# Performance work log

Measured on AMD Instinct MI355X. Metric: run time of the kernel, lower is better.

Reference implementation:

```python
import jax, jax.numpy as jnp
import numpy as np


def _forward(data_vecs, data_weights, data_biases, edge_weights, edge_biases,
             score_weights, data, types, graphs, edges, pos):
    data = np.asarray(data); types = np.asarray(types)
    graphs = np.asarray(graphs); edges = np.asarray(edges).copy()
    pos = int(pos)
    edges[pos] = -1  # forward() mutation: score the pos edge over ALL edge types
    n = int(data.shape[0]); G = int(graphs.shape[0]); dim = data_weights.shape[-1]

    # base (leaf) embeddings for all nodes at once: [n, dim]
    sel = data_vecs[types, data]  # [n, vec_dim] embedding-table gather
    base = jnp.einsum('nv,nvd->nd', sel, data_weights[types]) + data_biases[types]

    def add_child(emb, ce, e):
        # emb/ce: [dim] or [E, dim]; e < 0 -> broadcast child over all edge types
        if e < 0:
            contrib = jnp.einsum('d,edf->ef', ce, edge_weights) + edge_biases
        else:
            contrib = ce @ edge_weights[e] + edge_biases[e]
        return emb + contrib  # broadcasting [dim] + [E,dim] mirrors torch's cat-expand

    scores = []
    for g in range(G):
        parents = graphs[g].copy()
        roots = [i for i in range(n) if parents[i] == i]
        for i in range(len(roots) - 1):  # chain multiple roots (no-op for single root)
            parents[roots[i]] = roots[i + 1]
        root = roots[-1]
        parents[root] = -n
        children = {}
        for c in range(n):
            p = int(parents[c])
            if p >= 0:
                children.setdefault(p, []).append(c)
        denom = float(len(children) + 1)  # faithful to source: len of whole dict

        def rec(idx):
            emb = base[idx]
            if idx not in children:
                return emb
            for c in children[idx]:
                emb = add_child(emb, rec(c), int(edges[c]))
            return jnp.maximum(emb / denom, 0.0)

        emb = rec(root)
        final = add_child(jnp.zeros((dim,), base.dtype), emb, int(edges[root]))
        scores.append((final @ score_weights)[:, 0])  # [E]
    return jnp.stack(scores)  # [G, E]


def setup_inputs():
    T, V, VD, DIM, E = 2, 100000, 512, 512, 64
    N, G = 128, 16
    ks = jax.random.split(jax.random.key(0), 6)
    s = DIM ** -0.5  # keep recursion numerically stable (torch.rand init would overflow)
    inp = {
        'data_vecs': jax.random.normal(ks[0], (T, V, VD), jnp.float32),
        'data_weights': jax.random.uniform(ks[1], (T, VD, DIM), jnp.float32) * s,
        'data_biases': jax.random.uniform(ks[2], (T, DIM), jnp.float32) * s,
        'edge_weights': jax.random.uniform(ks[3], (E, DIM, DIM), jnp.float32) * s,
        'edge_biases': jax.random.uniform(ks[4], (E, DIM), jnp.float32) * s,
        'score_weights': jax.random.uniform(ks[5], (DIM, 1), jnp.float32) * s,
    }
    rng = np.random.RandomState(0)
    inp['data'] = rng.randint(0, V, size=N).astype(np.int64)
    inp['types'] = rng.randint(0, T, size=N).astype(np.int64)
    graphs = np.zeros((G, N), dtype=np.int64)
    for g in range(G):
        for i in range(1, N):
            graphs[g, i] = rng.randint(0, i)  # random tree; node 0 self-parent = root
    inp['graphs'] = graphs
    inp['edges'] = rng.randint(0, E, size=N).astype(np.int64)
    inp['pos'] = 5
    return inp


def reference(data_vecs, data_weights, data_biases, edge_weights, edge_biases,
              score_weights, data, types, graphs, edges, pos):
    return _forward(data_vecs, data_weights, data_biases, edge_weights,
                    edge_biases, score_weights, data, types, graphs, edges, pos)
```

## Files before the change

kernel.cpp:

```cpp
#include <hip/hip_runtime.h>

#define DIMC 512
#define NMAX 128

__global__ __launch_bounds__(256)
void base_kernel(const float* __restrict__ data_vecs,
                 const float* __restrict__ data_weights,
                 const float* __restrict__ data_biases,
                 const int* __restrict__ data,
                 const int* __restrict__ types,
                 float* __restrict__ base,
                 int V, int VD) {
  const int n = blockIdx.x;
  const int t = threadIdx.x;
  __shared__ float sel[DIMC];
  const int ty = types[n];
  const long long idx = data[n];
  const float* src = data_vecs + ((long long)ty * V + idx) * VD;
  for (int d = t; d < VD; d += 256) sel[d] = src[d];
  __syncthreads();
  const float* W = data_weights + (long long)ty * VD * DIMC;
  const int f0 = 2 * t;
  float2 a = {0.f, 0.f};
  for (int d = 0; d < VD; ++d) {
    const float s = sel[d];
    const float2 w = *(const float2*)(W + (long long)d * DIMC + f0);
    a.x = fmaf(s, w.x, a.x);
    a.y = fmaf(s, w.y, a.y);
  }
  const float* b = data_biases + (long long)ty * DIMC;
  base[(long long)n * DIMC + f0]     = a.x + b[f0];
  base[(long long)n * DIMC + f0 + 1] = a.y + b[f0 + 1];
}

__global__ __launch_bounds__(NMAX)
void setup_kernel(const int* __restrict__ graphs,
                  const int* __restrict__ edges,
                  const int* __restrict__ pos_p,
                  int* __restrict__ par, int* __restrict__ onp,
                  int* __restrict__ chOff, int* __restrict__ chList,
                  int* __restrict__ plist,
                  int* __restrict__ plen, int* __restrict__ eroot,
                  float* __restrict__ inv_denom,
                  int G, int N) {
  const int g = blockIdx.x;
  const int t = threadIdx.x;
  __shared__ int P[NMAX], C[NMAX], O[NMAX], CO[NMAX + 1];
  __shared__ int s_root;
  if (t < N) { P[t] = graphs[g * N + t]; C[t] = 0; O[t] = 0; }
  __syncthreads();
  if (t == 0) {
    int prev = -1;
    for (int i = 0; i < N; ++i)
      if (P[i] == i) { if (prev >= 0) P[prev] = i; prev = i; }
    s_root = prev;
    P[prev] = -1;
  }
  __syncthreads();
  const int root = s_root;
  if (t < N) { const int p = P[t]; if (p >= 0) atomicAdd(&C[p], 1); }
  __syncthreads();
  if (t == 0) {
    int internal = 0, acc = 0;
    for (int c = 0; c < N; ++c) {
      CO[c] = acc; acc += C[c];
      if (C[c] > 0) internal++;
    }
    CO[N] = acc;
    inv_denom[g] = 1.0f / (float)(internal + 1);
  }
  __syncthreads();
  if (t < N) {
    const int p = P[t];
    if (p >= 0) {
      int r = 0;
      for (int c = 0; c < t; ++c) if (P[c] == p) ++r;
      chList[g * N + CO[p] + r] = t;
    }
  }
  if (t == 0) {
    const int pos = *pos_p;
    int pl = 0;
    int x = (pos == root) ? -1 : P[pos];
    while (x >= 0) { plist[g * N + pl++] = x; O[x] = 1; x = P[x]; }
    plen[g] = pl;
    eroot[g] = (root == pos) ? -1 : edges[root];
  }
  __syncthreads();
  if (t < N) {
    par[g * N + t] = P[t];
    onp[g * N + t] = O[t];
    chOff[g * (N + 1) + t] = CO[t];
  }
  if (t == 0) chOff[g * (N + 1) + N] = CO[N];
}

__global__ __launch_bounds__(512)
void score_prep_kernel(const float* __restrict__ ew, const float* __restrict__ eb,
                       const float* __restrict__ sw_g,
                       const int* __restrict__ eroot,
                       float* __restrict__ u, float* __restrict__ c0) {
  const int g = blockIdx.x;
  const int t = threadIdx.x;
  __shared__ float sw[DIMC];
  __shared__ float red[DIMC];
  sw[t] = sw_g[t];
  __syncthreads();
  const int er = eroot[g];
  if (er < 0) { if (t == 0) c0[g] = 0.f; return; }
  const float* row = ew + (long long)er * DIMC * DIMC + (long long)t * DIMC;
  float a = 0.f;
  for (int f = 0; f < DIMC; ++f) a = fmaf(row[f], sw[f], a);
  u[(long long)g * DIMC + t] = a;
  red[t] = eb[(long long)er * DIMC + t] * sw[t];
  __syncthreads();
  for (int s = 256; s > 0; s >>= 1) {
    if (t < s) red[t] += red[t + s];
    __syncthreads();
  }
  if (t == 0) c0[g] = red[0];
}

__device__ __forceinline__ float agent_ld(const float* p) {
  return __hip_atomic_load((float*)p, __ATOMIC_RELAXED, __HIP_MEMORY_SCOPE_AGENT);
}
__device__ __forceinline__ void agent_st(float* p, float v) {
  __hip_atomic_store(p, v, __ATOMIC_RELAXED, __HIP_MEMORY_SCOPE_AGENT);
}

struct P1Args {
  const float* base; float* epos; float* contrib;
  const float* ew; const float* eb;
  const int* par; const int* onp;
  const int* chOff; const int* chList;
  const int* edges; const float* invd; const int* pos_p;
  int* ready;
  int G, N;
};

__global__ __launch_bounds__(128, 4)
void pass1_flags(P1Args p) {
  const int b = blockIdx.x;
  const int g = b / p.N;
  const int c = p.N - 1 - (b - g * p.N);
  const int gi = g * p.N + c;
  if (p.onp[gi]) return;
  const int t = threadIdx.x;
  const int f0 = 4 * t;
  __shared__ float v[DIMC];
  const int pos = *p.pos_p;
  const int pr = p.par[gi];
  const float inv = p.invd[g];
  const int cs   = p.chOff[g * (p.N + 1) + c];
  const int cend = p.chOff[g * (p.N + 1) + c + 1];

  if (cend > cs) {
    if (t == 0) {
      for (int k = cs; k < cend; ++k) {
        const int ch = p.chList[g * p.N + k];
        while (__hip_atomic_load(p.ready + (g * p.N + ch), __ATOMIC_RELAXED,
                                 __HIP_MEMORY_SCOPE_AGENT) == 0)
          __builtin_amdgcn_s_sleep(2);
      }
    }
    __syncthreads();
  }

  const float* bs = p.base + (long long)c * DIMC;
  float4 val = *(const float4*)(bs + f0);
  if (cend > cs) {
    for (int k = cs; k < cend; ++k) {
      const int ch = p.chList[g * p.N + k];
      const float* cv = p.contrib + ((long long)g * p.N + ch) * DIMC;
      val.x += agent_ld(cv + f0);
      val.y += agent_ld(cv + f0 + 1);
      val.z += agent_ld(cv + f0 + 2);
      val.w += agent_ld(cv + f0 + 3);
    }
    val.x = fmaxf(val.x * inv, 0.f);
    val.y = fmaxf(val.y * inv, 0.f);
    val.z = fmaxf(val.z * inv, 0.f);
    val.w = fmaxf(val.w * inv, 0.f);
  }
  if (c == pos)
    *(float4*)(p.epos + (long long)g * DIMC + f0) = val;
  v[f0] = val.x; v[f0 + 1] = val.y; v[f0 + 2] = val.z; v[f0 + 3] = val.w;
  __syncthreads();

  if (c != pos && pr >= 0) {
    const int e = p.edges[c];
    const float* W = p.ew + (long long)e * DIMC * DIMC;
    float4 a = {0.f, 0.f, 0.f, 0.f};
    #pragma unroll 8
    for (int d = 0; d < DIMC; ++d) {
      const float s = v[d];
      const float4 w = *(const float4*)(W + (long long)d * DIMC + f0);
      a.x = fmaf(s, w.x, a.x);
      a.y = fmaf(s, w.y, a.y);
      a.z = fmaf(s, w.z, a.z);
      a.w = fmaf(s, w.w, a.w);
    }
    const float4 bb = *(const float4*)(p.eb + (long long)e * DIMC + f0);
    float* cv = p.contrib + ((long long)g * p.N + c) * DIMC;
    agent_st(cv + f0,     a.x + bb.x);
    agent_st(cv + f0 + 1, a.y + bb.y);
    agent_st(cv + f0 + 2, a.z + bb.z);
    agent_st(cv + f0 + 3, a.w + bb.w);
  }
  __syncthreads();
  if (t == 0) {
    asm volatile("s_waitcnt vmcnt(0)" ::: "memory");
    __hip_atomic_store(p.ready + gi, 1, __ATOMIC_RELAXED,
                       __HIP_MEMORY_SCOPE_AGENT);
  }
}

struct P2Args {
  const float* base; const float* epos; const float* contrib;
  const float* ew; const float* eb; const float* sw;
  const float* u; const float* c0; const float* inv_denom;
  const int* plist; const int* plen; const int* edges; const int* pos_p;
  const int* chOff; const int* chList; const int* onp;
  float* out; int G, N, E;
};

__global__ __launch_bounds__(256)
void pass2_kernel(P2Args p) {
  const int g = blockIdx.x / p.E;
  const int e = blockIdx.x - g * p.E;
  const int t = threadIdx.x;
  const int f0 = 2 * t;
  __shared__ float ce[DIMC];
  __shared__ float red[256];
  const int pos = *p.pos_p;
  const float* es = p.epos + (long long)g * DIMC;
  ce[f0] = es[f0]; ce[f0 + 1] = es[f0 + 1];
  __syncthreads();
  const int pl = p.plen[g];
  const float inv = p.inv_denom[g];
  for (int s = 0; s < pl; ++s) {
    const int pnode = p.plist[g * p.N + s];
    const int we = (s == 0) ? e : p.edges[p.plist[g * p.N + s - 1]];
    const float* W = p.ew + (long long)we * DIMC * DIMC;
    float2 a = {0.f, 0.f};
    for (int d = 0; d < DIMC; ++d) {
      const float sv = ce[d];
      const float2 w = *(const float2*)(W + (long long)d * DIMC + f0);
      a.x = fmaf(sv, w.x, a.x);
      a.y = fmaf(sv, w.y, a.y);
    }
    a.x += p.eb[(long long)we * DIMC + f0];
    a.y += p.eb[(long long)we * DIMC + f0 + 1];
    const float* bs = p.base + (long long)pnode * DIMC;
    float sx = a.x + bs[f0];
    float sy = a.y + bs[f0 + 1];
    const int cs   = p.chOff[g * (p.N + 1) + pnode];
    const int cend = p.chOff[g * (p.N + 1) + pnode + 1];
    for (int k = cs; k < cend; ++k) {
      const int ch = p.chList[g * p.N + k];
      if (ch == pos || p.onp[g * p.N + ch]) continue;
      const float* cv = p.contrib + ((long long)g * p.N + ch) * DIMC;
      sx += cv[f0]; sy += cv[f0 + 1];
    }
    sx = fmaxf(sx * inv, 0.f);
    sy = fmaxf(sy * inv, 0.f);
    __syncthreads();
    ce[f0] = sx; ce[f0 + 1] = sy;
    __syncthreads();
  }
  float partial;
  if (pl > 0) {
    const float* ug = p.u + (long long)g * DIMC;
    partial = ce[f0] * ug[f0] + ce[f0 + 1] * ug[f0 + 1];
  } else {
    const float* W = p.ew + (long long)e * DIMC * DIMC;
    float2 a = {0.f, 0.f};
    for (int d = 0; d < DIMC; ++d) {
      const float sv = ce[d];
      const float2 w = *(const float2*)(W + (long long)d * DIMC + f0);
      a.x = fmaf(sv, w.x, a.x);
      a.y = fmaf(sv, w.y, a.y);
    }
    a.x += p.eb[(long long)e * DIMC + f0];
    a.y += p.eb[(long long)e * DIMC + f0 + 1];
    partial = a.x * p.sw[f0] + a.y * p.sw[f0 + 1];
  }
  red[t] = partial;
  __syncthreads();
  for (int s2 = 128; s2 > 0; s2 >>= 1) {
    if (t < s2) red[t] += red[t + s2];
    __syncthreads();
  }
  if (t == 0) {
    float res = red[0] + ((pl > 0) ? p.c0[g] : 0.f);
    p.out[(long long)g * p.E + e] = res;
  }
}

extern "C" void kernel_launch(void* const* d_in, const int* in_sizes, int n_in,
                              void* d_out, int out_size, void* d_ws, size_t ws_size,
                              hipStream_t stream) {
  const float* data_vecs    = (const float*)d_in[0];
  const float* data_weights = (const float*)d_in[1];
  const float* data_biases  = (const float*)d_in[2];
  const float* edge_weights = (const float*)d_in[3];
  const float* edge_biases  = (const float*)d_in[4];
  const float* score_w      = (const float*)d_in[5];
  const int*   data   = (const int*)d_in[6];
  const int*   types  = (const int*)d_in[7];
  const int*   graphs = (const int*)d_in[8];
  const int*   edges  = (const int*)d_in[9];
  const int*   pos_p  = (const int*)d_in[10];

  const int DIM = in_sizes[5];
  const int T   = in_sizes[2] / DIM;
  const int E   = in_sizes[4] / DIM;
  const int N   = in_sizes[6];
  const int G   = in_sizes[8] / N;
  const int VD  = in_sizes[1] / (T * DIM);
  const int V   = in_sizes[0] / (T * VD);
  (void)DIM; (void)n_in; (void)ws_size; (void)out_size;

  char* w = (char*)d_ws;
  float* base    = (float*)w;   w += (size_t)N * DIMC * sizeof(float);
  float* epos    = (float*)w;   w += (size_t)G * DIMC * sizeof(float);
  float* contrib = (float*)w;   w += (size_t)G * N * DIMC * sizeof(float);
  float* u       = (float*)w;   w += (size_t)G * DIMC * sizeof(float);
  float* c0      = (float*)w;   w += (size_t)G * sizeof(float);
  float* invd    = (float*)w;   w += (size_t)G * sizeof(float);
  int* par    = (int*)w;        w += (size_t)G * N * sizeof(int);
  int* onp    = (int*)w;        w += (size_t)G * N * sizeof(int);
  int* chOff  = (int*)w;        w += (size_t)G * (N + 1) * sizeof(int);
  int* chList = (int*)w;        w += (size_t)G * N * sizeof(int);
  int* plist  = (int*)w;        w += (size_t)G * N * sizeof(int);
  int* plen   = (int*)w;        w += (size_t)G * sizeof(int);
  int* eroot  = (int*)w;        w += (size_t)G * sizeof(int);
  int* ready  = (int*)w;        w += (size_t)G * N * sizeof(int);

  hipMemsetAsync(ready, 0, (size_t)G * N * sizeof(int), stream);

  base_kernel<<<N, 256, 0, stream>>>(data_vecs, data_weights, data_biases,
                                     data, types, base, V, VD);

  setup_kernel<<<G, NMAX, 0, stream>>>(graphs, edges, pos_p,
                                       par, onp, chOff, chList,
                                       plist, plen, eroot, invd, G, N);

  score_prep_kernel<<<G, 512, 0, stream>>>(edge_weights, edge_biases, score_w,
                                           eroot, u, c0);

  P1Args p1;
  p1.base = base; p1.epos = epos; p1.contrib = contrib;
  p1.ew = edge_weights; p1.eb = edge_biases;
  p1.par = par; p1.onp = onp;
  p1.chOff = chOff; p1.chList = chList;
  p1.edges = edges; p1.invd = invd; p1.pos_p = pos_p;
  p1.ready = ready;
  p1.G = G; p1.N = N;
  pass1_flags<<<G * N, 128, 0, stream>>>(p1);

  P2Args p2;
  p2.base = base; p2.epos = epos; p2.contrib = contrib;
  p2.ew = edge_weights; p2.eb = edge_biases; p2.sw = score_w;
  p2.u = u; p2.c0 = c0; p2.inv_denom = invd;
  p2.plist = plist; p2.plen = plen; p2.edges = edges; p2.pos_p = pos_p;
  p2.chOff = chOff; p2.chList = chList; p2.onp = onp;
  p2.out = (float*)d_out; p2.G = G; p2.N = N; p2.E = E;
  pass2_kernel<<<G * E, 256, 0, stream>>>(p2);
}
```

Before: 1.034 ms.

## Prefetch edge weights while waiting, split pass2 and score_prep across more threads

In pass1, idle threads warm the cache by touching the block's edge-weight matrix while thread 0 spins on child-ready flags, and stop once a shared flag is raised. Pass2 now uses 512 threads per block and splits the 512-long reduction dimension into four groups of 128 with float4 loads, combining partials through shared memory. score_prep is spread over 8x more blocks, with each wave computing row dot products via shuffle reductions and coalesced reads. Unroll pragmas are also raised. The cost is extra cache traffic from the prefetch and more shared memory and synchronisation per step.

```diff
diff --git a/kernel.cpp b/kernel.cpp
--- a/kernel.cpp
+++ b/kernel.cpp
@@ -22,6 +22,7 @@
   const float* W = data_weights + (long long)ty * VD * DIMC;
   const int f0 = 2 * t;
   float2 a = {0.f, 0.f};
+  #pragma unroll 16
   for (int d = 0; d < VD; ++d) {
     const float s = sel[d];
     const float2 w = *(const float2*)(W + (long long)d * DIMC + f0);
@@ -100,25 +101,39 @@
                        const float* __restrict__ sw_g,
                        const int* __restrict__ eroot,
                        float* __restrict__ u, float* __restrict__ c0) {
-  const int g = blockIdx.x;
+  const int g = blockIdx.x >> 3;
+  const int chunk = blockIdx.x & 7;
   const int t = threadIdx.x;
+  const int wave = t >> 6;
+  const int lane = t & 63;
   __shared__ float sw[DIMC];
-  __shared__ float red[DIMC];
   sw[t] = sw_g[t];
   __syncthreads();
   const int er = eroot[g];
-  if (er < 0) { if (t == 0) c0[g] = 0.f; return; }
-  const float* row = ew + (long long)er * DIMC * DIMC + (long long)t * DIMC;
-  float a = 0.f;
-  for (int f = 0; f < DIMC; ++f) a = fmaf(row[f], sw[f], a);
-  u[(long long)g * DIMC + t] = a;
-  red[t] = eb[(long long)er * DIMC + t] * sw[t];
-  __syncthreads();
-  for (int s = 256; s > 0; s >>= 1) {
-    if (t < s) red[t] += red[t + s];
-    __syncthreads();
-  }
-  if (t == 0) c0[g] = red[0];
+  if (er < 0) { if (t == 0 && chunk == 0) c0[g] = 0.f; return; }
+  const float* Wb = ew + (long long)er * DIMC * DIMC;
+  #pragma unroll
+  for (int rr = 0; rr < 8; ++rr) {
+    const int r = chunk * 64 + wave * 8 + rr;
+    const float* row = Wb + (long long)r * DIMC;
+    float a = 0.f;
+    #pragma unroll
+    for (int k = 0; k < 8; ++k)
+      a = fmaf(row[lane + 64 * k], sw[lane + 64 * k], a);
+    #pragma unroll
+    for (int off = 32; off > 0; off >>= 1) a += __shfl_down(a, off, 64);
+    if (lane == 0) u[(long long)g * DIMC + r] = a;
+  }
+  if (chunk == 0) {
+    __shared__ float red[512];
+    red[t] = eb[(long long)er * DIMC + t] * sw[t];
+    __syncthreads();
+    for (int s = 256; s > 0; s >>= 1) {
+      if (t < s) red[t] += red[t + s];
+      __syncthreads();
+    }
+    if (t == 0) c0[g] = red[0];
+  }
 }
 
 __device__ __forceinline__ float agent_ld(const float* p) {
@@ -148,13 +163,19 @@
   const int t = threadIdx.x;
   const int f0 = 4 * t;
   __shared__ float v[DIMC];
+  __shared__ int go;
   const int pos = *p.pos_p;
   const int pr = p.par[gi];
   const float inv = p.invd[g];
   const int cs   = p.chOff[g * (p.N + 1) + c];
   const int cend = p.chOff[g * (p.N + 1) + c + 1];
+  const bool will_mm = (c != pos && pr >= 0);
+  const int e = p.edges[c];
+  const float* W = p.ew + (long long)e * DIMC * DIMC;
 
   if (cend > cs) {
+    if (t == 0) go = 0;
+    __syncthreads();
     if (t == 0) {
       for (int k = cs; k < cend; ++k) {
         const int ch = p.chList[g * p.N + k];
@@ -162,6 +183,21 @@
                                  __HIP_MEMORY_SCOPE_AGENT) == 0)
           __builtin_amdgcn_s_sleep(2);
       }
+      __hip_atomic_store(&go, 1, __ATOMIC_RELAXED,
+                         __HIP_MEMORY_SCOPE_WORKGROUP);
+    } else if (t >= 64 && will_mm) {
+      float dummy = 0.f;
+      const int ti = t - 64;
+      for (int chunk = 0; chunk < 32; ++chunk) {
+        #pragma unroll
+        for (int k = 0; k < 8; ++k) {
+          const int line = chunk * 512 + k * 64 + ti;
+          dummy += W[(long long)line * 16];
+        }
+        if (__hip_atomic_load(&go, __ATOMIC_RELAXED,
+                              __HIP_MEMORY_SCOPE_WORKGROUP)) break;
+      }
+      asm volatile("" :: "v"(dummy));
     }
     __syncthreads();
   }
@@ -187,11 +223,9 @@
   v[f0] = val.x; v[f0 + 1] = val.y; v[f0 + 2] = val.z; v[f0 + 3] = val.w;
   __syncthreads();
 
-  if (c != pos && pr >= 0) {
-    const int e = p.edges[c];
-    const float* W = p.ew + (long long)e * DIMC * DIMC;
+  if (will_mm) {
     float4 a = {0.f, 0.f, 0.f, 0.f};
-    #pragma unroll 8
+    #pragma unroll 16
     for (int d = 0; d < DIMC; ++d) {
       const float s = v[d];
       const float4 w = *(const float4*)(W + (long long)d * DIMC + f0);
@@ -224,76 +258,90 @@
   float* out; int G, N, E;
 };
 
-__global__ __launch_bounds__(256)
+__global__ __launch_bounds__(512)
 void pass2_kernel(P2Args p) {
   const int g = blockIdx.x / p.E;
   const int e = blockIdx.x - g * p.E;
   const int t = threadIdx.x;
-  const int f0 = 2 * t;
+  const int dg = t >> 7;
+  const int tl = t & 127;
+  const int f0 = 4 * tl;
   __shared__ float ce[DIMC];
-  __shared__ float red[256];
+  __shared__ float part[4][DIMC];
+  __shared__ float red[512];
   const int pos = *p.pos_p;
-  const float* es = p.epos + (long long)g * DIMC;
-  ce[f0] = es[f0]; ce[f0 + 1] = es[f0 + 1];
+  ce[t] = p.epos[(long long)g * DIMC + t];
   __syncthreads();
   const int pl = p.plen[g];
   const float inv = p.inv_denom[g];
   for (int s = 0; s < pl; ++s) {
     const int pnode = p.plist[g * p.N + s];
     const int we = (s == 0) ? e : p.edges[p.plist[g * p.N + s - 1]];
-    const float* W = p.ew + (long long)we * DIMC * DIMC;
-    float2 a = {0.f, 0.f};
-    for (int d = 0; d < DIMC; ++d) {
-      const float sv = ce[d];
-      const float2 w = *(const float2*)(W + (long long)d * DIMC + f0);
+    const float* W = p.ew + (long long)we * DIMC * DIMC
+                   + (long long)(dg * 128) * DIMC;
+    float4 a = {0.f, 0.f, 0.f, 0.f};
+    #pragma unroll 16
+    for (int i = 0; i < 128; ++i) {
+      const float sv = ce[dg * 128 + i];
+      const float4 w = *(const float4*)(W + (long long)i * DIMC + f0);
       a.x = fmaf(sv, w.x, a.x);
       a.y = fmaf(sv, w.y, a.y);
-    }
-    a.x += p.eb[(long long)we * DIMC + f0];
-    a.y += p.eb[(long long)we * DIMC + f0 + 1];
-    const float* bs = p.base + (long long)pnode * DIMC;
-    float sx = a.x + bs[f0];
-    float sy = a.y + bs[f0 + 1];
+      a.z = fmaf(sv, w.z, a.z);
+      a.w = fmaf(sv, w.w, a.w);
+    }
+    part[dg][f0]     = a.x;
+    part[dg][f0 + 1] = a.y;
+    part[dg][f0 + 2] = a.z;
+    part[dg][f0 + 3] = a.w;
+    __syncthreads();
+    float sum = part[0][t] + part[1][t] + part[2][t] + part[3][t]
+              + p.eb[(long long)we * DIMC + t]
+              + p.base[(long long)pnode * DIMC + t];
     const int cs   = p.chOff[g * (p.N + 1) + pnode];
     const int cend = p.chOff[g * (p.N + 1) + pnode + 1];
     for (int k = cs; k < cend; ++k) {
       const int ch = p.chList[g * p.N + k];
       if (ch == pos || p.onp[g * p.N + ch]) continue;
-      const float* cv = p.contrib + ((long long)g * p.N + ch) * DIMC;
-      sx += cv[f0]; sy += cv[f0 + 1];
-    }
-    sx = fmaxf(sx * inv, 0.f);
-    sy = fmaxf(sy * inv, 0.f);
-    __syncthreads();
-    ce[f0] = sx; ce[f0 + 1] = sy;
+      sum += p.contrib[((long long)g * p.N + ch) * DIMC + t];
+    }
+    sum = fmaxf(sum * inv, 0.f);
+    __syncthreads();
+    ce[t] = sum;
     __syncthreads();
   }
   float partial;
   if (pl > 0) {
-    const float* ug = p.u + (long long)g * DIMC;
-    partial = ce[f0] * ug[f0] + ce[f0 + 1] * ug[f0 + 1];
+    partial = ce[t] * p.u[(long long)g * DIMC + t];
   } else {
-    const float* W = p.ew + (long long)e * DIMC * DIMC;
-    float2 a = {0.f, 0.f};
-    for (int d = 0; d < DIMC; ++d) {
-      const float sv = ce[d];
-      const float2 w = *(const float2*)(W + (long long)d * DIMC + f0);
+    const float* W = p.ew + (long long)e * DIMC * DIMC
+                   + (long long)(dg * 128) * DIMC;
+    float4 a = {0.f, 0.f, 0.f, 0.f};
+    #pragma unroll 16
+    for (int i = 0; i < 128; ++i) {
+      const float sv = ce[dg * 128 + i];
+      const float4 w = *(const float4*)(W + (long long)i * DIMC + f0);
       a.x = fmaf(sv, w.x, a.x);
       a.y = fmaf(sv, w.y, a.y);
-    }
-    a.x += p.eb[(long long)e * DIMC + f0];
-    a.y += p.eb[(long long)e * DIMC + f0 + 1];
-    partial = a.x * p.sw[f0] + a.y * p.sw[f0 + 1];
+      a.z = fmaf(sv, w.z, a.z);
+      a.w = fmaf(sv, w.w, a.w);
+    }
+    part[dg][f0]     = a.x;
+    part[dg][f0 + 1] = a.y;
+    part[dg][f0 + 2] = a.z;
+    part[dg][f0 + 3] = a.w;
+    __syncthreads();
+    const float fin = part[0][t] + part[1][t] + part[2][t] + part[3][t]
+                    + p.eb[(long long)e * DIMC + t];
+    partial = fin * p.sw[t];
   }
   red[t] = partial;
   __syncthreads();
-  for (int s2 = 128; s2 > 0; s2 >>= 1) {
+  for (int s2 = 256; s2 > 0; s2 >>= 1) {
     if (t < s2) red[t] += red[t + s2];
     __syncthreads();
   }
   if (t == 0) {
-    float res = red[0] + ((pl > 0) ? p.c0[g] : 0.f);
-    p.out[(long long)g * p.E + e] = res;
+    p.out[(long long)g * p.E + e] = red[0] + ((pl > 0) ? p.c0[g] : 0.f);
   }
 }
 
@@ -346,8 +394,8 @@
                                        par, onp, chOff, chList,
                                        plist, plen, eroot, invd, G, N);
 
-  score_prep_kernel<<<G, 512, 0, stream>>>(edge_weights, edge_biases, score_w,
-                                           eroot, u, c0);
+  score_prep_kernel<<<G * 8, 512, 0, stream>>>(edge_weights, edge_biases,
+                                               score_w, eroot, u, c0);
 
   P1Args p1;
   p1.base = base; p1.epos = epos; p1.contrib = contrib;
@@ -366,5 +414,5 @@
   p2.plist = plist; p2.plen = plen; p2.edges = edges; p2.pos_p = pos_p;
   p2.chOff = chOff; p2.chList = chList; p2.onp = onp;
   p2.out = (float*)d_out; p2.G = G; p2.N = N; p2.E = E;
-  pass2_kernel<<<G * E, 256, 0, stream>>>(p2);
-}
+  pass2_kernel<<<G * E, 512, 0, stream>>>(p2);
+}
```

New measurement: 980.3 us. 1.05x faster.
